# Kernel tuning notes

Hardware: AMD Instinct MI355X
Metric: run time of the kernel (lower is better)

The kernel has to match this reference:

```python
import jax, jax.numpy as jnp
import numpy as np

N = 100000   # total nodes (types a: [0,50000), b: [50000,100000))
E = 500000   # edges per edge type
T = 4        # number of edge types
D_IN = 128
H = 4        # heads
F = 32       # out_feats per head
NEG_SLOPE = 0.2


def setup_inputs() -> dict:
    key = jax.random.key(0)
    ks = jax.random.split(key, 8)
    feat = jax.random.normal(ks[0], (N, D_IN), dtype=jnp.float32)
    src = jax.random.randint(ks[1], (T, E), 0, N)
    dst = jax.random.randint(ks[2], (T, E), 0, N)
    is_b = jnp.arange(N) >= (N // 2)  # node-type mask (type2mask)
    W = jax.random.normal(ks[3], (T, D_IN, H * F), dtype=jnp.float32) * (1.0 / np.sqrt(D_IN))
    attn_l = jax.random.normal(ks[4], (T, H, F), dtype=jnp.float32) * 0.1
    attn_r = jax.random.normal(ks[5], (T, H, F), dtype=jnp.float32) * 0.1
    W_merge = jax.random.normal(ks[6], (2 * H * F, F), dtype=jnp.float32) * (1.0 / np.sqrt(2 * H * F))
    b_merge = jax.random.normal(ks[7], (F,), dtype=jnp.float32) * 0.01
    return {"feat": feat, "src": src, "dst": dst, "is_b": is_b,
            "W": W, "attn_l": attn_l, "attn_r": attn_r,
            "W_merge": W_merge, "b_merge": b_merge}


def _gat_etype(feat, src_t, dst_t, W_t, al_t, ar_t):
    # Projected features: [N, H, F]
    ft = (feat @ W_t).reshape(N, H, F)
    el = jnp.einsum('nhf,hf->nh', ft, al_t)  # [N, H]
    er = jnp.einsum('nhf,hf->nh', ft, ar_t)  # [N, H]
    # u_add_v then LeakyReLU: [E, H]
    e = el[src_t] + er[dst_t]
    e = jnp.where(e > 0, e, NEG_SLOPE * e)
    # edge_softmax over incoming edges of each dst node (stable)
    m = jax.lax.stop_gradient(jax.ops.segment_max(e, dst_t, num_segments=N))
    ex = jnp.exp(e - m[dst_t])
    denom = jax.ops.segment_sum(ex, dst_t, num_segments=N)
    a = ex / denom[dst_t]  # [E, H]
    # u_mul_e + scatter-sum: [N, H, F]
    msg = ft[src_t] * a[:, :, None]
    out = jax.ops.segment_sum(msg, dst_t, num_segments=N)
    return out.reshape(N, H * F)


def reference(feat, src, dst, is_b, W, attn_l, attn_r, W_merge, b_merge):
    outs = [_gat_etype(feat, src[t], dst[t], W[t], attn_l[t], attn_r[t])
            for t in range(T)]
    # etypes dst order: a, a, b, b -> two per-etype feats per dst ntype
    feat_a = jnp.concatenate([outs[0], outs[1]], axis=1) @ W_merge + b_merge  # [N, F]
    feat_b = jnp.concatenate([outs[2], outs[3]], axis=1) @ W_merge + b_merge  # [N, F]
    # base_aggr_func: start with type-a result, overwrite type-b rows
    return jnp.where(is_b[:, None], feat_b, feat_a)
```

## Files before the change

kernel.cpp:

```cpp
#include <hip/hip_runtime.h>

typedef short short8 __attribute__((ext_vector_type(8)));
typedef float f32x4 __attribute__((ext_vector_type(4)));

#define N_NODES 100000
#define N_A     50000
#define N_EDGES 500000
#define N_T     4
#define D_IN    128
#define HF      128
#define BCOLS   144
#define TN      (N_T * N_NODES)
#define TE      (N_T * N_EDGES)
#define NB1     ((TN + 1023) / 1024)
#define TILE_E  (BCOLS * D_IN)
#define LOG2E   1.44269504088896340736f

__device__ __forceinline__ unsigned short f2b(float f) {
  unsigned int u = __float_as_uint(f);
  u += 0x7FFFu + ((u >> 16) & 1u);
  return (unsigned short)(u >> 16);
}
__device__ __forceinline__ unsigned int pk2(float lo, float hi) {
  return (unsigned int)f2b(lo) | ((unsigned int)f2b(hi) << 16);
}
__device__ __forceinline__ float blo(unsigned int u) { return __uint_as_float(u << 16); }
__device__ __forceinline__ float bhi(unsigned int u) { return __uint_as_float(u & 0xFFFF0000u); }

__global__ __launch_bounds__(256) void k_prep(const float* __restrict__ W,
    const float* __restrict__ al, const float* __restrict__ ar,
    const float* __restrict__ Wm,
    unsigned short* __restrict__ Bt, unsigned short* __restrict__ WmT)
{
  if (blockIdx.x < 2) {
    int idx = blockIdx.x * 256 + threadIdx.x;
    int t = idx >> 7, k = idx & 127;
    const float* Wr = W + ((size_t)t * D_IN + k) * HF;
    unsigned short* o = Bt + (size_t)t * TILE_E;
    for (int j = 0; j < HF; ++j)
      o[(j * D_IN + k) ^ ((j & 7) << 3)] = f2b(Wr[j]);
    for (int h = 0; h < 4; ++h) {
      float sl = 0.f, sr = 0.f;
      const float* alh = al + (t * 4 + h) * 32;
      const float* arh = ar + (t * 4 + h) * 32;
      for (int f = 0; f < 32; ++f) { float w = Wr[h * 32 + f]; sl += w * alh[f]; sr += w * arh[f]; }
      int jl = 128 + h, jr = 132 + h;
      o[(jl * D_IN + k) ^ ((jl & 7) << 3)] = f2b(sl * LOG2E);
      o[(jr * D_IN + k) ^ ((jr & 7) << 3)] = f2b(sr * LOG2E);
    }
    for (int j = 136; j < 144; ++j)
      o[(j * D_IN + k) ^ ((j & 7) << 3)] = 0;
  } else {
    int idx = (blockIdx.x - 2) * 256 + threadIdx.x;
    int kidx = idx >> 5, j = idx & 31;
    int slot = kidx >> 7, p = kidx & 127;
    int col = (p & 7) * 16 + (p >> 3);
    WmT[j * 256 + kidx] = f2b(Wm[(slot * 128 + col) * 32 + j]);
  }
}

__global__ __launch_bounds__(256, 4) void k_proj(const float* __restrict__ feat,
    const unsigned short* __restrict__ Btg,
    unsigned short* __restrict__ ftg,
    float* __restrict__ elg, float* __restrict__ erg)
{
  __shared__ __align__(16) unsigned short Bs[TILE_E];
  const int tid = threadIdx.x;
  const int wave = tid >> 6, lane = tid & 63;
  const int l15 = lane & 15, g = lane >> 4;
  const int wrow0 = blockIdx.x * 64 + wave * 16;

  short8 a[4];
  {
    int row = wrow0 + l15;
    const float* fr = feat + (size_t)(row < N_NODES ? row : N_NODES - 1) * D_IN;
#pragma unroll
    for (int kt = 0; kt < 4; ++kt) {
      float4 v0 = *(const float4*)(fr + kt * 32 + g * 8);
      float4 v1 = *(const float4*)(fr + kt * 32 + g * 8 + 4);
      short8 s;
      s[0] = (short)f2b(v0.x); s[1] = (short)f2b(v0.y);
      s[2] = (short)f2b(v0.z); s[3] = (short)f2b(v0.w);
      s[4] = (short)f2b(v1.x); s[5] = (short)f2b(v1.y);
      s[6] = (short)f2b(v1.z); s[7] = (short)f2b(v1.w);
      a[kt] = s;
    }
  }

  for (int t = 0; t < N_T; ++t) {
    if (t > 0) __syncthreads();
    {
      const uint4* src = (const uint4*)(Btg + (size_t)t * TILE_E);
      uint4* dstv = (uint4*)Bs;
#pragma unroll
      for (int i = 0; i < 9; ++i)
        dstv[i * 256 + tid] = src[i * 256 + tid];
    }
    __syncthreads();

    f32x4 acc[8];
#pragma unroll
    for (int ct = 0; ct < 8; ++ct) {
      f32x4 c = {0.f, 0.f, 0.f, 0.f};
#pragma unroll
      for (int kt = 0; kt < 4; ++kt) {
        int row = ct * 16 + l15;
        int boff = (row * 256 + kt * 64 + g * 16) ^ ((l15 & 7) << 4);
        short8 b = *(const short8*)((const char*)Bs + boff);
        c = __builtin_amdgcn_mfma_f32_16x16x32_bf16(a[kt], b, c, 0, 0, 0);
      }
      acc[ct] = c;
    }
    {
      f32x4 c8 = {0.f, 0.f, 0.f, 0.f};
#pragma unroll
      for (int kt = 0; kt < 4; ++kt) {
        int row = 128 + l15;
        int boff = (row * 256 + kt * 64 + g * 16) ^ ((l15 & 7) << 4);
        short8 b = *(const short8*)((const char*)Bs + boff);
        c8 = __builtin_amdgcn_mfma_f32_16x16x32_bf16(a[kt], b, c8, 0, 0, 0);
      }
      if (l15 < 8) {
#pragma unroll
        for (int r = 0; r < 4; ++r) {
          int row = wrow0 + g * 4 + r;
          if (row < N_NODES) {
            float v = c8[r];
            if (l15 < 4) elg[((size_t)t * N_NODES + row) * 4 + l15] = v;
            else         erg[((size_t)t * N_NODES + row) * 4 + (l15 - 4)] = v;
          }
        }
      }
    }
#pragma unroll
    for (int r = 0; r < 4; ++r) {
      int row = wrow0 + g * 4 + r;
      if (row < N_NODES) {
        uint4 o;
        o.x = pk2(acc[0][r], acc[1][r]);
        o.y = pk2(acc[2][r], acc[3][r]);
        o.z = pk2(acc[4][r], acc[5][r]);
        o.w = pk2(acc[6][r], acc[7][r]);
        *(uint4*)(ftg + ((size_t)t * N_NODES + row) * HF + l15 * 8) = o;
      }
    }
  }
}

__global__ __launch_bounds__(256) void k_hist(const int* __restrict__ dst,
    int* __restrict__ cnt, int* __restrict__ rank) {
  int idx = blockIdx.x * 256 + threadIdx.x;
  if (idx >= TE) return;
  int t = idx / N_EDGES;
  int d = dst[idx];
  bool keep = (t < 2) ? (d < N_A) : (d >= N_A);
  if (keep) rank[idx] = atomicAdd(&cnt[t * N_NODES + d], 1);
}

__global__ __launch_bounds__(256) void k_scan1(const int* __restrict__ cnt,
    int* __restrict__ ofs, int* __restrict__ bsum) {
  __shared__ int ts[256];
  int b = blockIdx.x, t = threadIdx.x;
  int base = b * 1024 + t * 4;
  int v0 = 0, v1 = 0, v2 = 0, v3 = 0;
  if (base + 0 < TN) v0 = cnt[base + 0];
  if (base + 1 < TN) v1 = cnt[base + 1];
  if (base + 2 < TN) v2 = cnt[base + 2];
  if (base + 3 < TN) v3 = cnt[base + 3];
  int s = v0 + v1 + v2 + v3;
  ts[t] = s;
  __syncthreads();
  for (int o = 1; o < 256; o <<= 1) {
    int x = (t >= o) ? ts[t - o] : 0;
    __syncthreads();
    ts[t] += x;
    __syncthreads();
  }
  int run = ts[t] - s;
  if (base + 0 < TN) ofs[base + 0] = run; run += v0;
  if (base + 1 < TN) ofs[base + 1] = run; run += v1;
  if (base + 2 < TN) ofs[base + 2] = run; run += v2;
  if (base + 3 < TN) ofs[base + 3] = run;
  if (t == 255) bsum[b] = ts[255];
}

__global__ __launch_bounds__(512) void k_scan2(int* __restrict__ bsum) {
  __shared__ int ts[512];
  int t = threadIdx.x;
  int v = (t < NB1) ? bsum[t] : 0;
  ts[t] = v;
  __syncthreads();
  for (int o = 1; o < 512; o <<= 1) {
    int x = (t >= o) ? ts[t - o] : 0;
    __syncthreads();
    ts[t] += x;
    __syncthreads();
  }
  if (t < NB1) bsum[t] = ts[t] - v;
}

__global__ __launch_bounds__(256) void k_scatter(const int* __restrict__ src, const int* __restrict__ dst,
    const int* __restrict__ ofs, const int* __restrict__ bsum, const int* __restrict__ rank,
    int* __restrict__ bkt) {
  int idx = blockIdx.x * 256 + threadIdx.x;
  if (idx >= TE) return;
  int t = idx / N_EDGES;
  int d = dst[idx];
  bool keep = (t < 2) ? (d < N_A) : (d >= N_A);
  if (!keep) return;
  int key = t * N_NODES + d;
  int p = ofs[key] + bsum[key >> 10] + rank[idx];
  bkt[p] = t * N_NODES + src[idx];
}

__global__ __launch_bounds__(256) void k_gather(const int* __restrict__ bkt,
    const int* __restrict__ ofs, const int* __restrict__ cnt, const int* __restrict__ bsum,
    const float* __restrict__ elg, const float* __restrict__ erg,
    const uint4* __restrict__ ftu, uint4* __restrict__ aggb)
{
  int wid = blockIdx.x * 4 + (threadIdx.x >> 6);
  int lane = threadIdx.x & 63;
  int g8 = lane >> 3, l7 = lane & 7;
  int pid = wid * 8 + g8;
  int n = pid >> 1, slot = pid & 1;
  int t = slot + ((n >= N_A) ? 2 : 0);
  int key = t * N_NODES + n;
  int base = ofs[key] + bsum[key >> 10];
  int c = cnt[key];
  float4 er4 = *(const float4*)(erg + (size_t)key * 4);
  float a00 = 0.f, a01 = 0.f, a02 = 0.f, a03 = 0.f, a04 = 0.f, a05 = 0.f, a06 = 0.f, a07 = 0.f;
  float a10 = 0.f, a11 = 0.f, a12 = 0.f, a13 = 0.f, a14 = 0.f, a15 = 0.f, a16 = 0.f, a17 = 0.f;
  float d0 = 0.f, d1 = 0.f, d2 = 0.f, d3 = 0.f;
  int qb = l7 * 2;
  int i = 0;
  for (; i + 1 < c; i += 2) {
    int s0 = bkt[base + i];
    int s1 = bkt[base + i + 1];
    float4 el0 = *(const float4*)(elg + (size_t)s0 * 4);
    float4 el1 = *(const float4*)(elg + (size_t)s1 * 4);
    uint4 u0a = ftu[(size_t)s0 * 16 + qb];
    uint4 u0b = ftu[(size_t)s0 * 16 + qb + 1];
    uint4 u1a = ftu[(size_t)s1 * 16 + qb];
    uint4 u1b = ftu[(size_t)s1 * 16 + qb + 1];
    float s, w0, w1, w2, w3;
    s = el0.x + er4.x; w0 = exp2f(fmaxf(s, 0.2f * s));
    s = el0.y + er4.y; w1 = exp2f(fmaxf(s, 0.2f * s));
    s = el0.z + er4.z; w2 = exp2f(fmaxf(s, 0.2f * s));
    s = el0.w + er4.w; w3 = exp2f(fmaxf(s, 0.2f * s));
    d0 += w0; d1 += w1; d2 += w2; d3 += w3;
    a00 += w0 * blo(u0a.x); a01 += w0 * bhi(u0a.x);
    a02 += w1 * blo(u0a.y); a03 += w1 * bhi(u0a.y);
    a04 += w2 * blo(u0a.z); a05 += w2 * bhi(u0a.z);
    a06 += w3 * blo(u0a.w); a07 += w3 * bhi(u0a.w);
    a10 += w0 * blo(u0b.x); a11 += w0 * bhi(u0b.x);
    a12 += w1 * blo(u0b.y); a13 += w1 * bhi(u0b.y);
    a14 += w2 * blo(u0b.z); a15 += w2 * bhi(u0b.z);
    a16 += w3 * blo(u0b.w); a17 += w3 * bhi(u0b.w);
    s = el1.x + er4.x; w0 = exp2f(fmaxf(s, 0.2f * s));
    s = el1.y + er4.y; w1 = exp2f(fmaxf(s, 0.2f * s));
    s = el1.z + er4.z; w2 = exp2f(fmaxf(s, 0.2f * s));
    s = el1.w + er4.w; w3 = exp2f(fmaxf(s, 0.2f * s));
    d0 += w0; d1 += w1; d2 += w2; d3 += w3;
    a00 += w0 * blo(u1a.x); a01 += w0 * bhi(u1a.x);
    a02 += w1 * blo(u1a.y); a03 += w1 * bhi(u1a.y);
    a04 += w2 * blo(u1a.z); a05 += w2 * bhi(u1a.z);
    a06 += w3 * blo(u1a.w); a07 += w3 * bhi(u1a.w);
    a10 += w0 * blo(u1b.x); a11 += w0 * bhi(u1b.x);
    a12 += w1 * blo(u1b.y); a13 += w1 * bhi(u1b.y);
    a14 += w2 * blo(u1b.z); a15 += w2 * bhi(u1b.z);
    a16 += w3 * blo(u1b.w); a17 += w3 * bhi(u1b.w);
  }
  if (i < c) {
    int s0 = bkt[base + i];
    float4 el0 = *(const float4*)(elg + (size_t)s0 * 4);
    uint4 u0a = ftu[(size_t)s0 * 16 + qb];
    uint4 u0b = ftu[(size_t)s0 * 16 + qb + 1];
    float s, w0, w1, w2, w3;
    s = el0.x + er4.x; w0 = exp2f(fmaxf(s, 0.2f * s));
    s = el0.y + er4.y; w1 = exp2f(fmaxf(s, 0.2f * s));
    s = el0.z + er4.z; w2 = exp2f(fmaxf(s, 0.2f * s));
    s = el0.w + er4.w; w3 = exp2f(fmaxf(s, 0.2f * s));
    d0 += w0; d1 += w1; d2 += w2; d3 += w3;
    a00 += w0 * blo(u0a.x); a01 += w0 * bhi(u0a.x);
    a02 += w1 * blo(u0a.y); a03 += w1 * bhi(u0a.y);
    a04 += w2 * blo(u0a.z); a05 += w2 * bhi(u0a.z);
    a06 += w3 * blo(u0a.w); a07 += w3 * bhi(u0a.w);
    a10 += w0 * blo(u0b.x); a11 += w0 * bhi(u0b.x);
    a12 += w1 * blo(u0b.y); a13 += w1 * bhi(u0b.y);
    a14 += w2 * blo(u0b.z); a15 += w2 * bhi(u0b.z);
    a16 += w3 * blo(u0b.w); a17 += w3 * bhi(u0b.w);
  }
  float i0 = (c > 0) ? 1.f / d0 : 0.f;
  float i1 = (c > 0) ? 1.f / d1 : 0.f;
  float i2 = (c > 0) ? 1.f / d2 : 0.f;
  float i3 = (c > 0) ? 1.f / d3 : 0.f;
  uint4 oA, oB;
  oA.x = pk2(a00 * i0, a01 * i0);
  oA.y = pk2(a02 * i1, a03 * i1);
  oA.z = pk2(a04 * i2, a05 * i2);
  oA.w = pk2(a06 * i3, a07 * i3);
  oB.x = pk2(a10 * i0, a11 * i0);
  oB.y = pk2(a12 * i1, a13 * i1);
  oB.z = pk2(a14 * i2, a15 * i2);
  oB.w = pk2(a16 * i3, a17 * i3);
  size_t ob = (size_t)n * 32 + slot * 16 + qb;
  aggb[ob] = oA;
  aggb[ob + 1] = oB;
}

__global__ __launch_bounds__(256) void k_merge(const unsigned short* __restrict__ aggb,
    const unsigned short* __restrict__ WmT, const float* __restrict__ bm,
    float* __restrict__ out)
{
  __shared__ __align__(16) unsigned short Al[64 * 264];
  __shared__ __align__(16) unsigned short Bl[32 * 264];
  int n0 = blockIdx.x * 64;
  int tid = threadIdx.x;
  const uint4* asrc = (const uint4*)(aggb + (size_t)n0 * 256);
  for (int i = tid; i < 2048; i += 256) {
    int r = i >> 5, c = i & 31;
    *(uint4*)&Al[r * 264 + c * 8] = asrc[r * 32 + c];
  }
  for (int i = tid; i < 1024; i += 256) {
    int r = i >> 5, c = i & 31;
    *(uint4*)&Bl[r * 264 + c * 8] = ((const uint4*)WmT)[r * 32 + c];
  }
  __syncthreads();
  int wave = tid >> 6, lane = tid & 63;
  int l15 = lane & 15, lk = (lane >> 4) * 8;
  short8 a[8];
#pragma unroll
  for (int kt = 0; kt < 8; ++kt)
    a[kt] = *(const short8*)&Al[(wave * 16 + l15) * 264 + kt * 32 + lk];
  f32x4 acc0 = {0.f, 0.f, 0.f, 0.f}, acc1 = {0.f, 0.f, 0.f, 0.f};
#pragma unroll
  for (int kt = 0; kt < 8; ++kt) {
    short8 b0 = *(const short8*)&Bl[l15 * 264 + kt * 32 + lk];
    short8 b1 = *(const short8*)&Bl[(16 + l15) * 264 + kt * 32 + lk];
    acc0 = __builtin_amdgcn_mfma_f32_16x16x32_bf16(a[kt], b0, acc0, 0, 0, 0);
    acc1 = __builtin_amdgcn_mfma_f32_16x16x32_bf16(a[kt], b1, acc1, 0, 0, 0);
  }
  float bm0 = bm[l15], bm1 = bm[16 + l15];
#pragma unroll
  for (int r = 0; r < 4; ++r) {
    int row = n0 + wave * 16 + (lane >> 4) * 4 + r;
    if (row < N_NODES) {
      out[(size_t)row * 32 + l15] = acc0[r] + bm0;
      out[(size_t)row * 32 + 16 + l15] = acc1[r] + bm1;
    }
  }
}

extern "C" void kernel_launch(void* const* d_in, const int* in_sizes, int n_in,
                              void* d_out, int out_size, void* d_ws, size_t ws_size,
                              hipStream_t stream)
{
  const float* feat = (const float*)d_in[0];
  const int*   src  = (const int*)d_in[1];
  const int*   dst  = (const int*)d_in[2];
  const float* W    = (const float*)d_in[4];
  const float* al   = (const float*)d_in[5];
  const float* ar   = (const float*)d_in[6];
  const float* Wm   = (const float*)d_in[7];
  const float* bm   = (const float*)d_in[8];
  float* out = (float*)d_out;
  (void)in_sizes; (void)n_in; (void)out_size; (void)ws_size;

  char* w = (char*)d_ws;
  size_t o = 0;
  auto take = [&](size_t bytes) -> void* {
    void* p = w + o;
    o += (bytes + 255) & ~(size_t)255;
    return p;
  };
  unsigned short* Btg = (unsigned short*)take((size_t)N_T * TILE_E * 2);
  unsigned short* WmT = (unsigned short*)take((size_t)32 * 256 * 2);
  unsigned short* ftg = (unsigned short*)take((size_t)N_T * N_NODES * HF * 2);
  float* elg   = (float*)take((size_t)N_T * N_NODES * 4 * 4);
  float* erg   = (float*)take((size_t)N_T * N_NODES * 4 * 4);
  int*   cntb  = (int*)take((size_t)TN * 4);
  int*   ofs   = (int*)take((size_t)TN * 4);
  int*   bsum  = (int*)take(4096);
  int*   rank  = (int*)take((size_t)TE * 4);
  int*   bkt   = (int*)take((size_t)TE * 4);
  unsigned short* aggb = (unsigned short*)take((size_t)(N_NODES + 64) * 256 * 2);

  hipMemsetAsync(cntb, 0, (size_t)TN * 4, stream);

  k_prep<<<34, 256, 0, stream>>>(W, al, ar, Wm, Btg, WmT);
  k_proj<<<1563, 256, 0, stream>>>(feat, Btg, ftg, elg, erg);
  k_hist<<<(TE + 255) / 256, 256, 0, stream>>>(dst, cntb, rank);
  k_scan1<<<NB1, 256, 0, stream>>>(cntb, ofs, bsum);
  k_scan2<<<1, 512, 0, stream>>>(bsum);
  k_scatter<<<(TE + 255) / 256, 256, 0, stream>>>(src, dst, ofs, bsum, rank, bkt);
  k_gather<<<6250, 256, 0, stream>>>(bkt, ofs, cntb, bsum, elg, erg, (const uint4*)ftg, (uint4*)aggb);
  k_merge<<<1563, 256, 0, stream>>>(aggb, WmT, bm, out);
}
```

Measured before the change: 203.9 us.

## Sort destination node-etype pairs by in-degree before gather for load balance

Adds a counting sort (histogram, scan, scatter over three small kernels) that orders the (node, etype) pairs by incoming-edge count. The gather kernel then reads its pair id through this order array, so the eight pairs processed by each wavefront have similar degrees and lanes idle less in divergent loops. In exchange it adds three launches and two memsets, and it scatters the output writes and the el/er/ofs reads across nodes, which can hurt locality.

After: 240.2 us. 17.8% more time.

```diff
diff --git a/kernel.cpp b/kernel.cpp
--- a/kernel.cpp
+++ b/kernel.cpp
@@ -15,6 +15,8 @@
 #define NB1     ((TN + 1023) / 1024)
 #define TILE_E  (BCOLS * D_IN)
 #define LOG2E   1.44269504088896340736f
+#define PAIRS   (2 * N_NODES)
+#define NPBLK   ((PAIRS + 255) / 256)
 
 __device__ __forceinline__ unsigned short f2b(float f) {
   unsigned int u = __float_as_uint(f);
@@ -213,7 +215,62 @@
   bkt[p] = t * N_NODES + src[idx];
 }
 
-__global__ __launch_bounds__(256) void k_gather(const int* __restrict__ bkt,
+__global__ __launch_bounds__(256) void k_d1(const int* __restrict__ cnt, int* __restrict__ gdh) {
+  __shared__ int lh[64];
+  int tid = threadIdx.x;
+  if (tid < 64) lh[tid] = 0;
+  __syncthreads();
+  int pid = blockIdx.x * 256 + tid;
+  if (pid < PAIRS) {
+    int n = pid >> 1, slot = pid & 1;
+    int t = slot + ((n >= N_A) ? 2 : 0);
+    int c = cnt[t * N_NODES + n];
+    atomicAdd(&lh[c < 63 ? c : 63], 1);
+  }
+  __syncthreads();
+  if (tid < 64 && lh[tid]) atomicAdd(&gdh[tid], lh[tid]);
+}
+
+__global__ __launch_bounds__(64) void k_d2(const int* __restrict__ gdh, int* __restrict__ dbase) {
+  __shared__ int ts[64];
+  int t = threadIdx.x;
+  int v = gdh[t];
+  ts[t] = v;
+  __syncthreads();
+  for (int o = 1; o < 64; o <<= 1) {
+    int x = (t >= o) ? ts[t - o] : 0;
+    __syncthreads();
+    ts[t] += x;
+    __syncthreads();
+  }
+  dbase[t] = ts[t] - v;
+}
+
+__global__ __launch_bounds__(256) void k_d3(const int* __restrict__ cnt,
+    const int* __restrict__ dbase, int* __restrict__ dcur, int* __restrict__ order) {
+  __shared__ int lh[64];
+  __shared__ int lbase[64];
+  int tid = threadIdx.x;
+  if (tid < 64) lh[tid] = 0;
+  __syncthreads();
+  int pid = blockIdx.x * 256 + tid;
+  int bin = 0, lr = 0;
+  bool ok = pid < PAIRS;
+  if (ok) {
+    int n = pid >> 1, slot = pid & 1;
+    int t = slot + ((n >= N_A) ? 2 : 0);
+    int c = cnt[t * N_NODES + n];
+    bin = c < 63 ? c : 63;
+    lr = atomicAdd(&lh[bin], 1);
+  }
+  __syncthreads();
+  if (tid < 64) lbase[tid] = lh[tid] ? atomicAdd(&dcur[tid], lh[tid]) : 0;
+  __syncthreads();
+  if (ok) order[dbase[bin] + lbase[bin] + lr] = pid;
+}
+
+__global__ __launch_bounds__(256) void k_gather(const int* __restrict__ order,
+    const int* __restrict__ bkt,
     const int* __restrict__ ofs, const int* __restrict__ cnt, const int* __restrict__ bsum,
     const float* __restrict__ elg, const float* __restrict__ erg,
     const uint4* __restrict__ ftu, uint4* __restrict__ aggb)
@@ -221,7 +278,7 @@
   int wid = blockIdx.x * 4 + (threadIdx.x >> 6);
   int lane = threadIdx.x & 63;
   int g8 = lane >> 3, l7 = lane & 7;
-  int pid = wid * 8 + g8;
+  int pid = order[wid * 8 + g8];
   int n = pid >> 1, slot = pid & 1;
   int t = slot + ((n >= N_A) ? 2 : 0);
   int key = t * N_NODES + n;
@@ -383,9 +440,15 @@
   int*   bsum  = (int*)take(4096);
   int*   rank  = (int*)take((size_t)TE * 4);
   int*   bkt   = (int*)take((size_t)TE * 4);
+  int*   order = (int*)take((size_t)PAIRS * 4);
+  int*   gdh   = (int*)take(64 * 4);
+  int*   dbase = (int*)take(64 * 4);
+  int*   dcur  = (int*)take(64 * 4);
   unsigned short* aggb = (unsigned short*)take((size_t)(N_NODES + 64) * 256 * 2);
 
   hipMemsetAsync(cntb, 0, (size_t)TN * 4, stream);
+  hipMemsetAsync(gdh,  0, 64 * 4, stream);
+  hipMemsetAsync(dcur, 0, 64 * 4, stream);
 
   k_prep<<<34, 256, 0, stream>>>(W, al, ar, Wm, Btg, WmT);
   k_proj<<<1563, 256, 0, stream>>>(feat, Btg, ftg, elg, erg);
@@ -393,6 +456,9 @@
   k_scan1<<<NB1, 256, 0, stream>>>(cntb, ofs, bsum);
   k_scan2<<<1, 512, 0, stream>>>(bsum);
   k_scatter<<<(TE + 255) / 256, 256, 0, stream>>>(src, dst, ofs, bsum, rank, bkt);
-  k_gather<<<6250, 256, 0, stream>>>(bkt, ofs, cntb, bsum, elg, erg, (const uint4*)ftg, (uint4*)aggb);
+  k_d1<<<NPBLK, 256, 0, stream>>>(cntb, gdh);
+  k_d2<<<1, 64, 0, stream>>>(gdh, dbase);
+  k_d3<<<NPBLK, 256, 0, stream>>>(cntb, dbase, dcur, order);
+  k_gather<<<6250, 256, 0, stream>>>(order, bkt, ofs, cntb, bsum, elg, erg, (const uint4*)ftg, (uint4*)aggb);
   k_merge<<<1563, 256, 0, stream>>>(aggb, WmT, bm, out);
 }
```
